# Optimization experiments

Measured on AMD Instinct MI355X. Metric: run time of the kernel, lower is better.

The kernel has to match this reference:

```python
import jax, jax.numpy as jnp
import numpy as np

B, E, H, S, V, K = 128, 512, 512, 2048, 83, 3
PAD = 82


def _pos_emb(n, e):
    pos = jnp.arange(n, dtype=jnp.float32)[:, None]                      # [n,1]
    k = jnp.exp(-jnp.log(10000.0) * jnp.arange(0, e, 2, dtype=jnp.float32) / e)  # [e/2]
    arg = pos * k                                                        # [n,e/2]
    pe = jnp.stack([jnp.sin(arg), jnp.cos(arg)], axis=-1).reshape(n, e)  # interleave sin/cos
    return pe.T                                                          # [e,n]


def setup_inputs() -> dict:
    key = jax.random.key(0)
    ks = jax.random.split(key, 8)
    return {
        "encoder_output": jax.random.normal(ks[0], (B, H, S), dtype=jnp.float32),
        "encoder_total": jax.random.normal(ks[1], (B, H, S), dtype=jnp.float32),
        "decoder_input": jax.random.randint(ks[2], (B,), 0, V),
        "count": 0,
        "emb": jax.random.normal(ks[3], (V, E), dtype=jnp.float32) * 0.02,
        "conv_w": jax.random.normal(ks[4], (2 * H, E, K), dtype=jnp.float32) * 0.02,
        "conv_b": jnp.zeros((2 * H,), dtype=jnp.float32),
        "lin2_w": jax.random.normal(ks[5], (V, H), dtype=jnp.float32) * 0.02,
        "lin2_b": jnp.zeros((V,), dtype=jnp.float32),
    }


def reference(encoder_output, encoder_total, decoder_input, count, emb, conv_w, conv_b, lin2_w, lin2_b):
    # count==0 first-step path; dropout is identity (inference).
    pe3 = _pos_emb(K, E)                                    # [E,K]

    def layer(dec_in):
        # dec_in: [B,E,K]
        xp = dec_in + pe3[None]                             # positional embedding add
        y = jnp.einsum('bek,oek->bo', xp, conv_w) + conv_b  # valid conv1d, out length 1 -> [B,2H]
        a, b = jnp.split(y, 2, axis=1)
        glu = a * jax.nn.sigmoid(b)                         # [B,H]
        d = glu + xp[:, :, -1]                              # residual with last (pe-added) column
        scores = jnp.einsum('bh,bhs->bs', d, encoder_output)
        attn = jax.nn.softmax(scores, axis=-1)              # [B,S]
        c = jnp.einsum('bs,bhs->bh', attn, encoder_total)   # [B,H]
        h = glu + c
        logits = h @ lin2_w.T + lin2_b                      # [B,V]
        return h, jax.nn.log_softmax(logits, axis=-1)

    x = emb[decoder_input][:, :, None]                      # [B,E,1]
    pad_col = jnp.broadcast_to(emb[PAD][None, :, None], (B, E, 1))
    dec1 = jnp.concatenate([pad_col, pad_col, x], axis=2)   # [B,E,3]

    h1, _ = layer(dec1)                                     # n_l = 0
    dec2 = jnp.concatenate([dec1[:, :, :2], h1[:, :, None]], axis=2)
    h2, _ = layer(dec2)                                     # n_l = 1
    dec3 = jnp.concatenate([dec1[:, :, :2], h2[:, :, None]], axis=2)
    h3, ls3 = layer(dec3)                                   # n_l = 2

    return (jax.nn.softmax(h3, axis=1)[:, :, None],         # [B,H,1]
            ls3[:, None, :])                                # [B,1,V]
```

## Files before the change

### kernel.cpp

```cpp
#include <hip/hip_runtime.h>
#include <math.h>

#define B_   128
#define E_   512
#define H_   512
#define S_   2048
#define V_   83
#define PAD_ 82

__device__ __forceinline__ float pe_val(int e, int n) {
    float freq = expf(-9.210340371976184f * (float)(e & ~1) * (1.0f / 512.0f));
    float a = (float)n * freq;
    return (e & 1) ? cosf(a) : sinf(a);
}


__global__ void k_prep(const float* __restrict__ cw, float* __restrict__ W2t) {
    int idx = blockIdx.x * 256 + threadIdx.x;
    int e = idx >> 10, o = idx & 1023;
    W2t[idx] = cw[o * 1536 + e * 3 + 2];
}

__global__ void k_misc(const float* __restrict__ emb, float* __restrict__ pe2,
                       float* __restrict__ x01i) {
    int e = threadIdx.x;
    float freq = expf(-9.210340371976184f * (float)(e & ~1) * (1.0f / 512.0f));
    float p0 = (e & 1) ? 1.0f : 0.0f;
    float p1 = (e & 1) ? cosf(freq) : sinf(freq);
    float p2 = (e & 1) ? cosf(2.0f * freq) : sinf(2.0f * freq);
    pe2[e] = p2;
    float ep = emb[PAD_ * 512 + e];
    x01i[e * 3 + 0] = ep + p0;
    x01i[e * 3 + 1] = ep + p1;
    x01i[e * 3 + 2] = 0.0f;
}

__global__ void k_base3(const float* __restrict__ cw, const float* __restrict__ x01i,
                        float* __restrict__ base) {
    int t = threadIdx.x, w = t >> 6, lane = t & 63;
    __shared__ float xs[1536];
    for (int j = t; j < 1536; j += 256) xs[j] = x01i[j];
    __syncthreads();
    int o = blockIdx.x * 4 + w;
    const float* rp = cw + (size_t)o * 1536 + lane * 4;
    float acc = 0.f;
    #pragma unroll
    for (int j = 0; j < 6; ++j) {
        float4 v = *(const float4*)(rp + j * 256);
        const float* xp = &xs[lane * 4 + j * 256];
        acc += v.x * xp[0] + v.y * xp[1] + v.z * xp[2] + v.w * xp[3];
    }
    #pragma unroll
    for (int off = 32; off > 0; off >>= 1) acc += __shfl_down(acc, off, 64);
    if (lane == 0) base[o] = acc;
}


__global__ void k_x(int first, const int* __restrict__ tok, const float* __restrict__ emb,
                    const float* __restrict__ h, const float* __restrict__ pe2,
                    float* __restrict__ xcol) {
    int idx = blockIdx.x * 256 + threadIdx.x;
    int b = idx >> 9, e = idx & 511;
    float v = first ? emb[tok[b] * 512 + e] : h[idx];
    xcol[idx] = v + pe2[e];
}

__global__ void k_y(const float* __restrict__ xcol, const float* __restrict__ W2t,
                    const float* __restrict__ base, const float* __restrict__ cb,
                    float* __restrict__ y) {
    int oc = blockIdx.x, bq = blockIdx.y, t = threadIdx.x;
    __shared__ float xs[4][512];
    for (int j = t; j < 2048; j += 256) xs[j >> 9][j & 511] = xcol[bq * 2048 + j];
    __syncthreads();
    int o = oc * 256 + t;
    float init = base[o] + cb[o];
    float a0 = init, a1 = init, a2 = init, a3 = init;
    for (int e = 0; e < 512; ++e) {
        float w = W2t[e * 1024 + o];
        a0 += xs[0][e] * w; a1 += xs[1][e] * w;
        a2 += xs[2][e] * w; a3 += xs[3][e] * w;
    }
    int b0 = bq * 4;
    y[(size_t)(b0 + 0) * 1024 + o] = a0;
    y[(size_t)(b0 + 1) * 1024 + o] = a1;
    y[(size_t)(b0 + 2) * 1024 + o] = a2;
    y[(size_t)(b0 + 3) * 1024 + o] = a3;
}

__global__ void k_scores2(const float* __restrict__ y, const float* __restrict__ xcol,
                          const float* __restrict__ enc, float* __restrict__ part) {
    int hc = blockIdx.x, b = blockIdx.y, t = threadIdx.x;
    int w = t >> 6, lane = t & 63;
    __shared__ float dl[64];
    __shared__ float red[4 * 2048];
    if (t < 64) {
        int hg = hc * 64 + t;
        float ya = y[b * 1024 + hg];
        float yb_ = y[b * 1024 + 512 + hg];
        float g = ya / (1.0f + expf(-yb_));
        dl[t] = g + xcol[b * 512 + hg];
    }
    __syncthreads();
    float4 a[8];
    #pragma unroll
    for (int j = 0; j < 8; ++j) a[j] = make_float4(0.f, 0.f, 0.f, 0.f);
    const float* bp = enc + ((size_t)b * 512 + hc * 64 + w * 16) * 2048 + lane * 4;
    for (int r = 0; r < 16; ++r) {
        float dh = dl[w * 16 + r];
        const float* rp = bp + (size_t)r * 2048;
        #pragma unroll
        for (int j = 0; j < 8; ++j) {
            float4 v = *(const float4*)(rp + j * 256);
            a[j].x += dh * v.x; a[j].y += dh * v.y;
            a[j].z += dh * v.z; a[j].w += dh * v.w;
        }
    }
    #pragma unroll
    for (int j = 0; j < 8; ++j)
        *(float4*)&red[w * 2048 + j * 256 + lane * 4] = a[j];
    __syncthreads();
    #pragma unroll
    for (int k = 0; k < 2; ++k) {
        int s = t * 4 + k * 1024;
        float4 s0 = *(const float4*)&red[0 * 2048 + s];
        float4 s1 = *(const float4*)&red[1 * 2048 + s];
        float4 s2 = *(const float4*)&red[2 * 2048 + s];
        float4 s3 = *(const float4*)&red[3 * 2048 + s];
        float4 o4 = make_float4(s0.x + s1.x + s2.x + s3.x,
                                s0.y + s1.y + s2.y + s3.y,
                                s0.z + s1.z + s2.z + s3.z,
                                s0.w + s1.w + s2.w + s3.w);
        *(float4*)&part[(size_t)hc * 262144 + b * 2048 + s] = o4;
    }
}

__global__ void k_softmax2(const float* __restrict__ part, float* __restrict__ attn) {
    int b = blockIdx.x, t = threadIdx.x;
    float v[8];
    float m = -1e30f;
    for (int i = 0; i < 8; ++i) {
        int s = i * 256 + t;
        float acc = 0.f;
        #pragma unroll
        for (int hc = 0; hc < 8; ++hc) acc += part[(size_t)hc * 262144 + b * 2048 + s];
        v[i] = acc; m = fmaxf(m, acc);
    }
    __shared__ float r[256];
    r[t] = m; __syncthreads();
    for (int s = 128; s > 0; s >>= 1) { if (t < s) r[t] = fmaxf(r[t], r[t + s]); __syncthreads(); }
    float M = r[0]; __syncthreads();
    float sum = 0.f;
    for (int i = 0; i < 8; ++i) { v[i] = expf(v[i] - M); sum += v[i]; }
    r[t] = sum; __syncthreads();
    for (int s = 128; s > 0; s >>= 1) { if (t < s) r[t] += r[t + s]; __syncthreads(); }
    float inv = 1.0f / r[0];
    for (int i = 0; i < 8; ++i) attn[b * 2048 + i * 256 + t] = v[i] * inv;
}

__global__ void k_c2(const float* __restrict__ attn, const float* __restrict__ enc,
                     const float* __restrict__ y, float* __restrict__ hbuf) {
    int t = threadIdx.x;
    int widx = blockIdx.x * 4 + (t >> 6);
    int lane = t & 63;
    int b = widx >> 9, hh = widx & 511;
    const float* vp = enc + (size_t)(b * 512 + hh) * 2048;
    const float* ap = attn + b * 2048;
    float acc = 0.f;
    #pragma unroll
    for (int it = 0; it < 8; ++it) {
        int s = it * 256 + lane * 4;
        float4 w = *(const float4*)(vp + s);
        float4 p = *(const float4*)(ap + s);
        acc += p.x * w.x + p.y * w.y + p.z * w.z + p.w * w.w;
    }
    #pragma unroll
    for (int off = 32; off > 0; off >>= 1) acc += __shfl_down(acc, off, 64);
    if (lane == 0) {
        float ya = y[b * 1024 + hh];
        float yb_ = y[b * 1024 + 512 + hh];
        float g = ya / (1.0f + expf(-yb_));
        hbuf[b * 512 + hh] = g + acc;
    }
}


__global__ void k_logits(const float* __restrict__ h, const float* __restrict__ l2w,
                         const float* __restrict__ l2b, float* __restrict__ out) {
    int b = blockIdx.x, t = threadIdx.x;
    __shared__ float hl[512];
    for (int j = t; j < 512; j += 128) hl[j] = h[b * 512 + j];
    __syncthreads();
    float acc = 0.f;
    if (t < V_) {
        acc = l2b[t];
        for (int e = 0; e < 512; ++e) acc += hl[e] * l2w[t * 512 + e];
    }
    __shared__ float r[128];
    r[t] = (t < V_) ? acc : -1e30f; __syncthreads();
    for (int s = 64; s > 0; s >>= 1) { if (t < s) r[t] = fmaxf(r[t], r[t + s]); __syncthreads(); }
    float M = r[0]; __syncthreads();
    r[t] = (t < V_) ? expf(acc - M) : 0.f; __syncthreads();
    for (int s = 64; s > 0; s >>= 1) { if (t < s) r[t] += r[t + s]; __syncthreads(); }
    float L = M + logf(r[0]);
    if (t < V_) out[65536 + b * V_ + t] = acc - L;
}

__global__ void k_out0(const float* __restrict__ h, float* __restrict__ out) {
    int b = blockIdx.x, t = threadIdx.x;
    float v0 = h[b * 512 + t], v1 = h[b * 512 + 256 + t];
    __shared__ float r[256];
    r[t] = fmaxf(v0, v1); __syncthreads();
    for (int s = 128; s > 0; s >>= 1) { if (t < s) r[t] = fmaxf(r[t], r[t + s]); __syncthreads(); }
    float M = r[0]; __syncthreads();
    float e0 = expf(v0 - M), e1 = expf(v1 - M);
    r[t] = e0 + e1; __syncthreads();
    for (int s = 128; s > 0; s >>= 1) { if (t < s) r[t] += r[t + s]; __syncthreads(); }
    float inv = 1.0f / r[0];
    out[b * 512 + t] = e0 * inv;
    out[b * 512 + 256 + t] = e1 * inv;
}


extern "C" void kernel_launch(void* const* d_in, const int* in_sizes, int n_in,
                              void* d_out, int out_size, void* d_ws, size_t ws_size,
                              hipStream_t stream) {
    const float* enc_out = (const float*)d_in[0];
    const float* enc_tot = (const float*)d_in[1];
    const int*   tok     = (const int*)d_in[2];
    const float* emb     = (const float*)d_in[4];
    const float* conv_w  = (const float*)d_in[5];
    const float* conv_b  = (const float*)d_in[6];
    const float* l2w     = (const float*)d_in[7];
    const float* l2b     = (const float*)d_in[8];
    float* out = (float*)d_out;
    float* ws = (float*)d_ws;

    float* W2t  = ws;
    float* base = W2t + 524288;
    float* pe2  = base + 1024;
    float* x01i = pe2 + 512;
    float* xcol = x01i + 1536;
    float* yb   = xcol + 65536;
    float* attn = yb + 131072;
    float* part = attn + 262144;
    float* hbuf = part + 2097152;

    k_prep<<<2048, 256, 0, stream>>>(conv_w, W2t);
    k_misc<<<1, 512, 0, stream>>>(emb, pe2, x01i);
    k_base3<<<256, 256, 0, stream>>>(conv_w, x01i, base);

    for (int L = 0; L < 3; ++L) {
        k_x<<<256, 256, 0, stream>>>(L == 0 ? 1 : 0, tok, emb, hbuf, pe2, xcol);
        k_y<<<dim3(4, 32), 256, 0, stream>>>(xcol, W2t, base, conv_b, yb);
        k_scores2<<<dim3(8, 128), 256, 0, stream>>>(yb, xcol, enc_out, part);
        k_softmax2<<<128, 256, 0, stream>>>(part, attn);
        k_c2<<<16384, 256, 0, stream>>>(attn, enc_tot, yb, hbuf);
    }

    k_logits<<<128, 128, 0, stream>>>(hbuf, l2w, l2b, out);
    k_out0<<<128, 256, 0, stream>>>(hbuf, out);
}
```

Measured before the change: 706.2 us.

## Fuse x-prep into conv GEMV, tile weight transpose, use nontemporal encoder loads

Folds the per-layer x-column kernel into the conv GEMV kernel, and merges the logits and output-softmax kernels into one epilogue, removing launches. The conv-weight transpose now goes through a shared-memory tile so reads and writes are both coalesced. Encoder tensor streams in the scores and context kernels use nontemporal loads, and the context kernel stages attention weights in LDS, to reduce cache pollution and redundant global reads. Each of the four k_yx blocks per batch group recomputes the x-column, and only oc==0 writes it back to global memory.

```diff
diff --git a/kernel.cpp b/kernel.cpp
--- a/kernel.cpp
+++ b/kernel.cpp
@@ -8,18 +8,12 @@
 #define V_   83
 #define PAD_ 82
 
-__device__ __forceinline__ float pe_val(int e, int n) {
-    float freq = expf(-9.210340371976184f * (float)(e & ~1) * (1.0f / 512.0f));
-    float a = (float)n * freq;
-    return (e & 1) ? cosf(a) : sinf(a);
-}
-
-
-__global__ void k_prep(const float* __restrict__ cw, float* __restrict__ W2t) {
-    int idx = blockIdx.x * 256 + threadIdx.x;
-    int e = idx >> 10, o = idx & 1023;
-    W2t[idx] = cw[o * 1536 + e * 3 + 2];
-}
+typedef float v4f __attribute__((ext_vector_type(4)));
+
+__device__ __forceinline__ v4f ldnt4(const float* p) {
+    return __builtin_nontemporal_load((const v4f*)p);
+}
+
 
 __global__ void k_misc(const float* __restrict__ emb, float* __restrict__ pe2,
                        float* __restrict__ x01i) {
@@ -55,23 +49,38 @@
     if (lane == 0) base[o] = acc;
 }
 
-
-__global__ void k_x(int first, const int* __restrict__ tok, const float* __restrict__ emb,
-                    const float* __restrict__ h, const float* __restrict__ pe2,
-                    float* __restrict__ xcol) {
-    int idx = blockIdx.x * 256 + threadIdx.x;
-    int b = idx >> 9, e = idx & 511;
-    float v = first ? emb[tok[b] * 512 + e] : h[idx];
-    xcol[idx] = v + pe2[e];
-}
-
-__global__ void k_y(const float* __restrict__ xcol, const float* __restrict__ W2t,
-                    const float* __restrict__ base, const float* __restrict__ cb,
-                    float* __restrict__ y) {
+__global__ void k_prep(const float* __restrict__ cw, float* __restrict__ W2t) {
+    __shared__ float tile[64][129];
+    int ob = blockIdx.x * 64, eb = blockIdx.y * 128;
+    int t = threadIdx.x;
+    for (int idx = t; idx < 8192; idx += 256) {
+        int r = idx >> 7, e = idx & 127;
+        tile[r][e] = cw[(size_t)(ob + r) * 1536 + (eb + e) * 3 + 2];
+    }
+    __syncthreads();
+    for (int idx = t; idx < 8192; idx += 256) {
+        int e = idx >> 6, o = idx & 63;
+        W2t[(size_t)(eb + e) * 1024 + ob + o] = tile[o][e];
+    }
+}
+
+
+__global__ void k_yx(int first, const int* __restrict__ tok, const float* __restrict__ emb,
+                     const float* __restrict__ h, const float* __restrict__ pe2,
+                     const float* __restrict__ W2t, const float* __restrict__ base,
+                     const float* __restrict__ cb, float* __restrict__ xcol,
+                     float* __restrict__ y) {
     int oc = blockIdx.x, bq = blockIdx.y, t = threadIdx.x;
     __shared__ float xs[4][512];
-    for (int j = t; j < 2048; j += 256) xs[j >> 9][j & 511] = xcol[bq * 2048 + j];
-    __syncthreads();
+    for (int j = t; j < 2048; j += 256) {
+        int bb = j >> 9, e = j & 511;
+        int b = bq * 4 + bb;
+        float v = first ? emb[tok[b] * 512 + e] : h[b * 512 + e];
+        xs[bb][e] = v + pe2[e];
+    }
+    __syncthreads();
+    if (oc == 0)
+        for (int j = t; j < 2048; j += 256) xcol[bq * 2048 + j] = xs[j >> 9][j & 511];
     int o = oc * 256 + t;
     float init = base[o] + cb[o];
     float a0 = init, a1 = init, a2 = init, a3 = init;
@@ -101,36 +110,31 @@
         dl[t] = g + xcol[b * 512 + hg];
     }
     __syncthreads();
-    float4 a[8];
-    #pragma unroll
-    for (int j = 0; j < 8; ++j) a[j] = make_float4(0.f, 0.f, 0.f, 0.f);
+    v4f a[8];
+    #pragma unroll
+    for (int j = 0; j < 8; ++j) a[j] = (v4f)(0.f);
     const float* bp = enc + ((size_t)b * 512 + hc * 64 + w * 16) * 2048 + lane * 4;
     for (int r = 0; r < 16; ++r) {
         float dh = dl[w * 16 + r];
         const float* rp = bp + (size_t)r * 2048;
         #pragma unroll
         for (int j = 0; j < 8; ++j) {
-            float4 v = *(const float4*)(rp + j * 256);
-            a[j].x += dh * v.x; a[j].y += dh * v.y;
-            a[j].z += dh * v.z; a[j].w += dh * v.w;
+            v4f v = ldnt4(rp + j * 256);
+            a[j] += dh * v;
         }
     }
     #pragma unroll
     for (int j = 0; j < 8; ++j)
-        *(float4*)&red[w * 2048 + j * 256 + lane * 4] = a[j];
+        *(v4f*)&red[w * 2048 + j * 256 + lane * 4] = a[j];
     __syncthreads();
     #pragma unroll
     for (int k = 0; k < 2; ++k) {
         int s = t * 4 + k * 1024;
-        float4 s0 = *(const float4*)&red[0 * 2048 + s];
-        float4 s1 = *(const float4*)&red[1 * 2048 + s];
-        float4 s2 = *(const float4*)&red[2 * 2048 + s];
-        float4 s3 = *(const float4*)&red[3 * 2048 + s];
-        float4 o4 = make_float4(s0.x + s1.x + s2.x + s3.x,
-                                s0.y + s1.y + s2.y + s3.y,
-                                s0.z + s1.z + s2.z + s3.z,
-                                s0.w + s1.w + s2.w + s3.w);
-        *(float4*)&part[(size_t)hc * 262144 + b * 2048 + s] = o4;
+        v4f s0 = *(const v4f*)&red[0 * 2048 + s];
+        v4f s1 = *(const v4f*)&red[1 * 2048 + s];
+        v4f s2 = *(const v4f*)&red[2 * 2048 + s];
+        v4f s3 = *(const v4f*)&red[3 * 2048 + s];
+        *(v4f*)&part[(size_t)hc * 262144 + b * 2048 + s] = (s0 + s1) + (s2 + s3);
     }
 }
 
@@ -160,18 +164,21 @@
 __global__ void k_c2(const float* __restrict__ attn, const float* __restrict__ enc,
                      const float* __restrict__ y, float* __restrict__ hbuf) {
     int t = threadIdx.x;
-    int widx = blockIdx.x * 4 + (t >> 6);
-    int lane = t & 63;
-    int b = widx >> 9, hh = widx & 511;
-    const float* vp = enc + (size_t)(b * 512 + hh) * 2048;
-    const float* ap = attn + b * 2048;
+    int b  = blockIdx.x >> 7;
+    int h0 = (blockIdx.x & 127) << 2;
+    __shared__ float al[2048];
+    for (int j = t; j < 2048; j += 256) al[j] = attn[b * 2048 + j];
+    __syncthreads();
+    int w = t >> 6, lane = t & 63;
+    int hh = h0 + w;
+    const float* vp = enc + ((size_t)b * 512 + hh) * 2048;
     float acc = 0.f;
     #pragma unroll
     for (int it = 0; it < 8; ++it) {
         int s = it * 256 + lane * 4;
-        float4 w = *(const float4*)(vp + s);
-        float4 p = *(const float4*)(ap + s);
-        acc += p.x * w.x + p.y * w.y + p.z * w.z + p.w * w.w;
+        v4f v = ldnt4(vp + s);
+        float4 p = *(const float4*)&al[s];
+        acc += p.x * v[0] + p.y * v[1] + p.z * v[2] + p.w * v[3];
     }
     #pragma unroll
     for (int off = 32; off > 0; off >>= 1) acc += __shfl_down(acc, off, 64);
@@ -184,35 +191,31 @@
 }
 
 
-__global__ void k_logits(const float* __restrict__ h, const float* __restrict__ l2w,
-                         const float* __restrict__ l2b, float* __restrict__ out) {
+__global__ void k_epi(const float* __restrict__ h, const float* __restrict__ l2w,
+                      const float* __restrict__ l2b, float* __restrict__ out) {
     int b = blockIdx.x, t = threadIdx.x;
     __shared__ float hl[512];
-    for (int j = t; j < 512; j += 128) hl[j] = h[b * 512 + j];
+    hl[t] = h[b * 512 + t]; hl[t + 256] = h[b * 512 + 256 + t];
     __syncthreads();
     float acc = 0.f;
     if (t < V_) {
         acc = l2b[t];
         for (int e = 0; e < 512; ++e) acc += hl[e] * l2w[t * 512 + e];
     }
-    __shared__ float r[128];
+    __shared__ float r[256];
     r[t] = (t < V_) ? acc : -1e30f; __syncthreads();
-    for (int s = 64; s > 0; s >>= 1) { if (t < s) r[t] = fmaxf(r[t], r[t + s]); __syncthreads(); }
+    for (int s = 128; s > 0; s >>= 1) { if (t < s) r[t] = fmaxf(r[t], r[t + s]); __syncthreads(); }
     float M = r[0]; __syncthreads();
     r[t] = (t < V_) ? expf(acc - M) : 0.f; __syncthreads();
-    for (int s = 64; s > 0; s >>= 1) { if (t < s) r[t] += r[t + s]; __syncthreads(); }
+    for (int s = 128; s > 0; s >>= 1) { if (t < s) r[t] += r[t + s]; __syncthreads(); }
     float L = M + logf(r[0]);
     if (t < V_) out[65536 + b * V_ + t] = acc - L;
-}
-
-__global__ void k_out0(const float* __restrict__ h, float* __restrict__ out) {
-    int b = blockIdx.x, t = threadIdx.x;
-    float v0 = h[b * 512 + t], v1 = h[b * 512 + 256 + t];
-    __shared__ float r[256];
+    __syncthreads();
+    float v0 = hl[t], v1 = hl[t + 256];
     r[t] = fmaxf(v0, v1); __syncthreads();
     for (int s = 128; s > 0; s >>= 1) { if (t < s) r[t] = fmaxf(r[t], r[t + s]); __syncthreads(); }
-    float M = r[0]; __syncthreads();
-    float e0 = expf(v0 - M), e1 = expf(v1 - M);
+    float M2 = r[0]; __syncthreads();
+    float e0 = expf(v0 - M2), e1 = expf(v1 - M2);
     r[t] = e0 + e1; __syncthreads();
     for (int s = 128; s > 0; s >>= 1) { if (t < s) r[t] += r[t + s]; __syncthreads(); }
     float inv = 1.0f / r[0];
@@ -245,18 +248,17 @@
     float* part = attn + 262144;
     float* hbuf = part + 2097152;
 
-    k_prep<<<2048, 256, 0, stream>>>(conv_w, W2t);
     k_misc<<<1, 512, 0, stream>>>(emb, pe2, x01i);
     k_base3<<<256, 256, 0, stream>>>(conv_w, x01i, base);
+    k_prep<<<dim3(16, 4), 256, 0, stream>>>(conv_w, W2t);
 
     for (int L = 0; L < 3; ++L) {
-        k_x<<<256, 256, 0, stream>>>(L == 0 ? 1 : 0, tok, emb, hbuf, pe2, xcol);
-        k_y<<<dim3(4, 32), 256, 0, stream>>>(xcol, W2t, base, conv_b, yb);
+        k_yx<<<dim3(4, 32), 256, 0, stream>>>(L == 0 ? 1 : 0, tok, emb, hbuf, pe2,
+                                              W2t, base, conv_b, xcol, yb);
         k_scores2<<<dim3(8, 128), 256, 0, stream>>>(yb, xcol, enc_out, part);
         k_softmax2<<<128, 256, 0, stream>>>(part, attn);
         k_c2<<<16384, 256, 0, stream>>>(attn, enc_tot, yb, hbuf);
     }
 
-    k_logits<<<128, 128, 0, stream>>>(hbuf, l2w, l2b, out);
-    k_out0<<<128, 256, 0, stream>>>(hbuf, out);
-}
+    k_epi<<<128, 256, 0, stream>>>(hbuf, l2w, l2b, out);
+}
```

New measurement: 630.2 us. -10.8%, faster.
